# Optimization experiments

Hardware: AMD Instinct MI355X
Metric: run time of the kernel (lower is better)

The kernel has to match this reference:

```python
import jax, jax.numpy as jnp
import numpy as np


def setup_inputs() -> dict:
    key = jax.random.key(0)
    k1, k2, k3, k4 = jax.random.split(key, 4)
    T, D, N = 8192, 128, 32
    x = jax.random.normal(k1, (T, D), dtype=jnp.float32)
    h_a0 = jax.random.normal(k2, (N, D), dtype=jnp.float32)
    h_sd0 = jax.random.uniform(k3, (N, D), dtype=jnp.float32)
    alpha = jax.random.uniform(k4, (N, D), dtype=jnp.float32)  # nn.Parameter uniform(0,1)
    return {"x": x, "h_a0": h_a0, "h_sd0": h_sd0, "alpha": alpha}


def reference(x, h_a0, h_sd0, alpha):
    # EMA with standard deviation (with_SD=True), expressed as a lax.scan
    # over the time axis. h state: (h_a, h_v) each (num_N, input_dim).
    h_v0 = h_sd0 ** 2

    def step(carry, x_i):
        h_a, h_v = carry
        d = x_i[None, :] - h_a            # (N, D)
        h_v = (1.0 - alpha) * (h_v + alpha * d * d)
        h_a = h_a + alpha * d
        return (h_a, h_v), (h_a, h_v)

    (hN_a, hN_v), (out_a, out_v) = jax.lax.scan(step, (h_a0, h_v0), x)
    # out_a/out_v: (T, N, D); torch code concatenates avg and sqrt(var) on dim 1
    out = jnp.concatenate([out_a, jnp.sqrt(out_v)], axis=1)  # (T, 2N, D)
    return out, hN_a, jnp.sqrt(hN_v)
```

## Files before the change

### kernel.cpp

```cpp
#include <hip/hip_runtime.h>
#include <math.h>

typedef float vf4 __attribute__((ext_vector_type(4)));

constexpr int T = 8192;
constexpr int D = 128;
constexpr int N = 32;
constexpr int L = 32;
constexpr int LOG2L = 5;
constexpr int K = T / L;
constexpr int S = N * D;
constexpr int S4 = S / 4;
constexpr int D4 = D / 4;
constexpr int OSTRIDE4 = (2 * N * D) / 4;

constexpr int SEG  = 8;
constexpr int CPS  = K / SEG;
constexpr int LOG2CPS = 5;
constexpr int COLS = 32;

__device__ __forceinline__ float fast_sqrt(float x) {
    float r;
    asm("v_sqrt_f32 %0, %1" : "=v"(r) : "v"(x));
    return r;
}

__global__ __launch_bounds__(256) void k1_summaries(
    const vf4* __restrict__ x, const vf4* __restrict__ alpha,
    vf4* __restrict__ c_a, vf4* __restrict__ cA, vf4* __restrict__ cP)
{
    int gid = blockIdx.x * 256 + threadIdx.x;
    int k   = gid >> 10;
    int s4  = gid & (S4 - 1);
    int d4  = s4 & (D4 - 1);

    vf4 a = alpha[s4];
    vf4 b = 1.0f - a;
    vf4 q = {0.f, 0.f, 0.f, 0.f};
    vf4 A = {0.f, 0.f, 0.f, 0.f};
    vf4 P = {0.f, 0.f, 0.f, 0.f};
    const vf4* xp = x + (size_t)k * L * D4 + d4;
#pragma unroll 8
    for (int i = 0; i < L; ++i) {
        vf4 xv = xp[(size_t)i * D4];
        vf4 p  = xv - q;
        P += p;
        A = b * (A + (a * p) * p);
        q = q + a * p;
    }
    c_a[gid] = q;
    cA[gid]  = A;
    cP[gid]  = P;
}

__global__ __launch_bounds__(256) void k2_scan(
    const vf4* __restrict__ h_a0, const vf4* __restrict__ h_sd0,
    const vf4* __restrict__ alpha,
    vf4* __restrict__ buf0,
    vf4* __restrict__ buf1,
    const vf4* __restrict__ buf2,
    float* __restrict__ out)
{
    __shared__ vf4 Cagg[SEG][COLS];
    __shared__ vf4 Vagg[SEG][COLS];

    int t   = threadIdx.x;
    int col = t & (COLS - 1);
    int kg  = t >> 5;
    int s4  = blockIdx.x * COLS + col;
    int kbase = kg * CPS;

    vf4 a = alpha[s4];
    vf4 b = 1.0f - a;
    vf4 bl = b;
#pragma unroll
    for (int i = 0; i < LOG2L; ++i) bl *= bl;
    vf4 M = bl;
#pragma unroll
    for (int i = 0; i < LOG2CPS; ++i) M *= M;
    vf4 Cq = bl * (1.0f - bl);
    vf4 Bc = a * bl;

    vf4 C = {0.f, 0.f, 0.f, 0.f};
#pragma unroll 4
    for (int j = 0; j < CPS; ++j)
        C = bl * C + buf0[(size_t)(kbase + j) * S4 + s4];
    Cagg[kg][col] = C;
    __syncthreads();

    vf4 H = h_a0[s4];
    for (int g = 0; g < kg; ++g) H = M * H + Cagg[g][col];

    vf4 Vg = {0.f, 0.f, 0.f, 0.f};
#pragma unroll 4
    for (int j = 0; j < CPS; ++j) {
        size_t idx = (size_t)(kbase + j) * S4 + s4;
        vf4 ca = buf0[idx];
        vf4 Ak = buf1[idx];
        vf4 Pk = buf2[idx];
        buf0[idx] = H;
        vf4 cv = Ak - 2.0f * ((Bc * Pk) * H) + Cq * (H * H);
        Vg = bl * Vg + cv;
        H  = bl * H + ca;
    }
    Vagg[kg][col] = Vg;
    if (kg == SEG - 1) {
        ((vf4*)(out + (size_t)T * 2 * N * D))[s4] = H;
    }
    __syncthreads();

    vf4 sdv = h_sd0[s4];
    vf4 V = sdv * sdv;
    for (int g = 0; g < kg; ++g) V = M * V + Vagg[g][col];

#pragma unroll 4
    for (int j = 0; j < CPS; ++j) {
        size_t idx = (size_t)(kbase + j) * S4 + s4;
        vf4 Hk = buf0[idx];
        vf4 Ak = buf1[idx];
        vf4 Pk = buf2[idx];
        vf4 Vc;
#pragma unroll
        for (int jj = 0; jj < 4; ++jj) Vc[jj] = fmaxf(V[jj], 0.f);
        buf1[idx] = Vc;
        vf4 cv = Ak - 2.0f * ((Bc * Pk) * Hk) + Cq * (Hk * Hk);
        V = bl * Vc + cv;
    }
    if (kg == SEG - 1) {
        vf4 r;
#pragma unroll
        for (int jj = 0; jj < 4; ++jj) r[jj] = fast_sqrt(fmaxf(V[jj], 0.f));
        ((vf4*)(out + (size_t)T * 2 * N * D))[S4 + s4] = r;
    }
}

__global__ __launch_bounds__(256) void k3_rows(
    const vf4* __restrict__ x, const vf4* __restrict__ alpha,
    const vf4* __restrict__ h_a_start, const vf4* __restrict__ h_v_start,
    vf4* __restrict__ out)
{
    const int k   = blockIdx.x;
    const int tid = threadIdx.x;
    const int d4  = tid & (D4 - 1);

    vf4 a[4], b[4], h[4], v[4];
#pragma unroll
    for (int j = 0; j < 4; ++j) {
        int s4 = tid + 256 * j;
        a[j] = alpha[s4];
        b[j] = 1.0f - a[j];
        h[j] = h_a_start[(size_t)k * S4 + s4];
        v[j] = h_v_start[(size_t)k * S4 + s4];
    }

    const vf4* xp   = x + (size_t)k * L * D4 + d4;
    vf4*       orow = out + (size_t)k * L * OSTRIDE4;

    for (int i = 0; i < L; ++i) {
        vf4 xv = xp[(size_t)i * D4];
#pragma unroll
        for (int j = 0; j < 4; ++j) {
            vf4 dx  = xv - h[j];
            vf4 adx = a[j] * dx;
            v[j] = b[j] * (v[j] + adx * dx);
            h[j] = h[j] + adx;
            vf4 r;
#pragma unroll
            for (int jj = 0; jj < 4; ++jj) r[jj] = fast_sqrt(v[j][jj]);
            orow[tid + 256 * j]        = h[j];
            orow[1024 + tid + 256 * j] = r;
        }
        orow += OSTRIDE4;
    }
}

extern "C" void kernel_launch(void* const* d_in, const int* in_sizes, int n_in,
                              void* d_out, int out_size, void* d_ws, size_t ws_size,
                              hipStream_t stream) {
    const vf4* x     = (const vf4*)d_in[0];
    const vf4* h_a0  = (const vf4*)d_in[1];
    const vf4* h_sd0 = (const vf4*)d_in[2];
    const vf4* alpha = (const vf4*)d_in[3];
    float* out = (float*)d_out;
    float* ws  = (float*)d_ws;

    vf4* buf0 = (vf4*)(ws + 0 * (size_t)K * S);
    vf4* buf1 = (vf4*)(ws + 1 * (size_t)K * S);
    vf4* buf2 = (vf4*)(ws + 2 * (size_t)K * S);

    dim3 blk(256);

    k1_summaries<<<dim3(K * S4 / 256), blk, 0, stream>>>(x, alpha, buf0, buf1, buf2);
    k2_scan<<<dim3(S4 / COLS), blk, 0, stream>>>(h_a0, h_sd0, alpha,
                                                 buf0, buf1, buf2, out);
    k3_rows<<<dim3(K), blk, 0, stream>>>(x, alpha, buf0, buf1, (vf4*)out);
}
```

Measured before the change: 298.2 us.

## Fuse chunk summary computation into scan kernel using shared-memory summaries

```diff
diff --git a/kernel.cpp b/kernel.cpp
--- a/kernel.cpp
+++ b/kernel.cpp
@@ -14,10 +14,10 @@
 constexpr int D4 = D / 4;
 constexpr int OSTRIDE4 = (2 * N * D) / 4;
 
-constexpr int SEG  = 8;
+constexpr int COLS = 4;
+constexpr int SEG  = 64;
 constexpr int CPS  = K / SEG;
-constexpr int LOG2CPS = 5;
-constexpr int COLS = 32;
+constexpr int LOG2CPS = 2;
 
 __device__ __forceinline__ float fast_sqrt(float x) {
     float r;
@@ -25,50 +25,23 @@
     return r;
 }
 
-__global__ __launch_bounds__(256) void k1_summaries(
-    const vf4* __restrict__ x, const vf4* __restrict__ alpha,
-    vf4* __restrict__ c_a, vf4* __restrict__ cA, vf4* __restrict__ cP)
-{
-    int gid = blockIdx.x * 256 + threadIdx.x;
-    int k   = gid >> 10;
-    int s4  = gid & (S4 - 1);
-    int d4  = s4 & (D4 - 1);
-
-    vf4 a = alpha[s4];
-    vf4 b = 1.0f - a;
-    vf4 q = {0.f, 0.f, 0.f, 0.f};
-    vf4 A = {0.f, 0.f, 0.f, 0.f};
-    vf4 P = {0.f, 0.f, 0.f, 0.f};
-    const vf4* xp = x + (size_t)k * L * D4 + d4;
-#pragma unroll 8
-    for (int i = 0; i < L; ++i) {
-        vf4 xv = xp[(size_t)i * D4];
-        vf4 p  = xv - q;
-        P += p;
-        A = b * (A + (a * p) * p);
-        q = q + a * p;
-    }
-    c_a[gid] = q;
-    cA[gid]  = A;
-    cP[gid]  = P;
-}
-
-__global__ __launch_bounds__(256) void k2_scan(
-    const vf4* __restrict__ h_a0, const vf4* __restrict__ h_sd0,
-    const vf4* __restrict__ alpha,
-    vf4* __restrict__ buf0,
-    vf4* __restrict__ buf1,
-    const vf4* __restrict__ buf2,
+__global__ __launch_bounds__(256) void kA_sumscan(
+    const vf4* __restrict__ x, const vf4* __restrict__ h_a0,
+    const vf4* __restrict__ h_sd0, const vf4* __restrict__ alpha,
+    vf4* __restrict__ h_a_start, vf4* __restrict__ h_v_start,
     float* __restrict__ out)
 {
+    __shared__ vf4 Qs[K][COLS];
+    __shared__ vf4 As[K][COLS];
+    __shared__ vf4 Ps[K][COLS];
     __shared__ vf4 Cagg[SEG][COLS];
     __shared__ vf4 Vagg[SEG][COLS];
 
-    int t   = threadIdx.x;
-    int col = t & (COLS - 1);
-    int kg  = t >> 5;
-    int s4  = blockIdx.x * COLS + col;
-    int kbase = kg * CPS;
+    const int t   = threadIdx.x;
+    const int col = t & (COLS - 1);
+    const int kg  = t >> 2;
+    const int s4  = blockIdx.x * COLS + col;
+    const int d4  = s4 & (D4 - 1);
 
     vf4 a = alpha[s4];
     vf4 b = 1.0f - a;
@@ -82,9 +55,25 @@
     vf4 Bc = a * bl;
 
     vf4 C = {0.f, 0.f, 0.f, 0.f};
-#pragma unroll 4
-    for (int j = 0; j < CPS; ++j)
-        C = bl * C + buf0[(size_t)(kbase + j) * S4 + s4];
+    for (int kk = 0; kk < CPS; ++kk) {
+        const int kglob = kg * CPS + kk;
+        const vf4* xp = x + (size_t)kglob * L * D4 + d4;
+        vf4 q = {0.f, 0.f, 0.f, 0.f};
+        vf4 A = {0.f, 0.f, 0.f, 0.f};
+        vf4 P = {0.f, 0.f, 0.f, 0.f};
+#pragma unroll 8
+        for (int i = 0; i < L; ++i) {
+            vf4 xv = xp[(size_t)i * D4];
+            vf4 p  = xv - q;
+            P += p;
+            A = b * (A + (a * p) * p);
+            q = q + a * p;
+        }
+        Qs[kglob][col] = q;
+        As[kglob][col] = A;
+        Ps[kglob][col] = P;
+        C = bl * C + q;
+    }
     Cagg[kg][col] = C;
     __syncthreads();
 
@@ -92,13 +81,12 @@
     for (int g = 0; g < kg; ++g) H = M * H + Cagg[g][col];
 
     vf4 Vg = {0.f, 0.f, 0.f, 0.f};
-#pragma unroll 4
-    for (int j = 0; j < CPS; ++j) {
-        size_t idx = (size_t)(kbase + j) * S4 + s4;
-        vf4 ca = buf0[idx];
-        vf4 Ak = buf1[idx];
-        vf4 Pk = buf2[idx];
-        buf0[idx] = H;
+    for (int kk = 0; kk < CPS; ++kk) {
+        const int kglob = kg * CPS + kk;
+        vf4 ca = Qs[kglob][col];
+        vf4 Ak = As[kglob][col];
+        vf4 Pk = Ps[kglob][col];
+        h_a_start[(size_t)kglob * S4 + s4] = H;
         vf4 cv = Ak - 2.0f * ((Bc * Pk) * H) + Cq * (H * H);
         Vg = bl * Vg + cv;
         H  = bl * H + ca;
@@ -113,18 +101,20 @@
     vf4 V = sdv * sdv;
     for (int g = 0; g < kg; ++g) V = M * V + Vagg[g][col];
 
-#pragma unroll 4
-    for (int j = 0; j < CPS; ++j) {
-        size_t idx = (size_t)(kbase + j) * S4 + s4;
-        vf4 Hk = buf0[idx];
-        vf4 Ak = buf1[idx];
-        vf4 Pk = buf2[idx];
+    vf4 H2 = h_a0[s4];
+    for (int g = 0; g < kg; ++g) H2 = M * H2 + Cagg[g][col];
+    for (int kk = 0; kk < CPS; ++kk) {
+        const int kglob = kg * CPS + kk;
+        vf4 ca = Qs[kglob][col];
+        vf4 Ak = As[kglob][col];
+        vf4 Pk = Ps[kglob][col];
         vf4 Vc;
 #pragma unroll
         for (int jj = 0; jj < 4; ++jj) Vc[jj] = fmaxf(V[jj], 0.f);
-        buf1[idx] = Vc;
-        vf4 cv = Ak - 2.0f * ((Bc * Pk) * Hk) + Cq * (Hk * Hk);
-        V = bl * Vc + cv;
+        h_v_start[(size_t)kglob * S4 + s4] = Vc;
+        vf4 cv = Ak - 2.0f * ((Bc * Pk) * H2) + Cq * (H2 * H2);
+        V  = bl * Vc + cv;
+        H2 = bl * H2 + ca;
     }
     if (kg == SEG - 1) {
         vf4 r;
@@ -184,14 +174,13 @@
     float* out = (float*)d_out;
     float* ws  = (float*)d_ws;
 
-    vf4* buf0 = (vf4*)(ws + 0 * (size_t)K * S);
-    vf4* buf1 = (vf4*)(ws + 1 * (size_t)K * S);
-    vf4* buf2 = (vf4*)(ws + 2 * (size_t)K * S);
+    vf4* h_a_start = (vf4*)(ws + 0 * (size_t)K * S);
+    vf4* h_v_start = (vf4*)(ws + 1 * (size_t)K * S);
 
     dim3 blk(256);
 
-    k1_summaries<<<dim3(K * S4 / 256), blk, 0, stream>>>(x, alpha, buf0, buf1, buf2);
-    k2_scan<<<dim3(S4 / COLS), blk, 0, stream>>>(h_a0, h_sd0, alpha,
-                                                 buf0, buf1, buf2, out);
-    k3_rows<<<dim3(K), blk, 0, stream>>>(x, alpha, buf0, buf1, (vf4*)out);
+    kA_sumscan<<<dim3(S4 / COLS), blk, 0, stream>>>(x, h_a0, h_sd0, alpha,
+                                                    h_a_start, h_v_start, out);
+    k3_rows<<<dim3(K), blk, 0, stream>>>(x, alpha, h_a_start, h_v_start,
+                                         (vf4*)out);
 }
```

Measured after the change: 289.6 us. 2.9% less time.
